# Kernel tuning notes

Measured on AMD Instinct MI355X. Metric: run time of the kernel, lower is better.

The kernel has to match this reference:

```python
import jax, jax.numpy as jnp
import numpy as np

NUM_USERS = 100000
USER_EMB_DIM = 64
PROC_DIM = 128          # Dense(128) embedding_processor
NUM_SHARDS = 16
MEM_SIZE = 512          # memory slots per shard
WORD_SIZE = 64
NUM_READS = 4
INPUT_SIZE = 256
B, S = 256, 128
IN_DIM = INPUT_SIZE + PROC_DIM  # combined controller input width


def setup_inputs() -> dict:
    key = jax.random.key(0)
    k = jax.random.split(key, 7)
    x = jax.random.normal(k[0], (B, S, INPUT_SIZE), dtype=jnp.float32)
    user_id = jax.random.randint(k[1], (B,), 0, NUM_USERS, dtype=jnp.int64)
    user_emb_table = jax.random.normal(k[2], (NUM_USERS, USER_EMB_DIM), dtype=jnp.float32) * 0.02
    W_proc = jax.random.normal(k[3], (USER_EMB_DIM, PROC_DIM), dtype=jnp.float32) * (1.0 / np.sqrt(USER_EMB_DIM))
    b_proc = jnp.zeros((PROC_DIM,), dtype=jnp.float32)
    # per-shard parameters: query projection + memory matrix (the shard's state)
    Wq = jax.random.normal(k[4], (NUM_SHARDS, IN_DIM, NUM_READS * WORD_SIZE), dtype=jnp.float32) * (1.0 / np.sqrt(IN_DIM))
    memory = jax.random.normal(k[5], (NUM_SHARDS, MEM_SIZE, WORD_SIZE), dtype=jnp.float32)
    return {"x": x, "user_id": user_id, "user_emb_table": user_emb_table,
            "W_proc": W_proc, "b_proc": b_proc, "Wq": Wq, "memory": memory}


def reference(x, user_id, user_emb_table, W_proc, b_proc, Wq, memory):
    # user embedding lookup + Dense processor
    ue = user_emb_table[user_id]                       # [B, E]
    pe = ue @ W_proc + b_proc                          # [B, PROC_DIM]
    # broadcast the processed embedding across the sequence and concat on features
    pe_seq = jnp.broadcast_to(pe[:, None, :], (x.shape[0], x.shape[1], pe.shape[-1]))
    combined = jnp.concatenate([x, pe_seq], axis=-1)   # [B, S, IN_DIM]
    # shard routing (irregular gather of per-shard params)
    sid = user_id % NUM_SHARDS                         # [B]
    Wq_g = Wq[sid]                                     # [B, IN_DIM, R*W]
    mem_g = memory[sid]                                # [B, M, W]
    # per-sample shard forward: content-based read
    q = jnp.einsum('bsi,bio->bso', combined, Wq_g)     # [B, S, R*W]
    q = q.reshape(q.shape[0], q.shape[1], NUM_READS, WORD_SIZE)
    scores = jnp.einsum('bsrw,bmw->bsrm', q, mem_g)    # [B, S, R, M]
    wts = jax.nn.softmax(scores, axis=-1)
    read_words = jnp.einsum('bsrm,bmw->bsrw', wts, mem_g)  # [B, S, R, W]
    # original code keeps final_states[-1] (last sample's state)
    final_state = wts[-1]                              # [S, R, M]
    return read_words, final_state
```

## Files before the change

### kernel.cpp

```cpp
#include <hip/hip_runtime.h>
#include <math.h>

#define BB 256
#define SSEQ 128
#define INPUT 256
#define PD 128
#define EE 64
#define RW 256
#define MM 512
#define WW 64
#define KD 384

typedef _Float16 half8 __attribute__((ext_vector_type(8)));
typedef __fp16 fp16x2 __attribute__((ext_vector_type(2)));
typedef float float4v __attribute__((ext_vector_type(4)));
typedef float f32x16 __attribute__((ext_vector_type(16)));
typedef unsigned int uint2v __attribute__((ext_vector_type(2)));

#define LOG2E 1.44269504088896f
#define OUT1 8388608u

#define MEMT16   4096
#define F32_OFF  131072
#define LDS_BYTES (131072 + 6144)
#define UE_O 0
#define PE_O 64
#define QPE_O 192
#define QP_O 448

union H8 { half8 h8; unsigned int u[4]; uint4 u4; };

__device__ __forceinline__ unsigned int pk2(float a, float b) {
    union { fp16x2 h; unsigned int u; } p;
    p.h = __builtin_amdgcn_cvt_pkrtz(a, b);
    return p.u;
}

__device__ __forceinline__ float xhalf_max(float v) {
    uint2v r = __builtin_amdgcn_permlane32_swap(__float_as_uint(v), __float_as_uint(v), false, false);
    return fmaxf(__uint_as_float(r[0]), __uint_as_float(r[1]));
}
__device__ __forceinline__ float xhalf_sum(float v) {
    uint2v r = __builtin_amdgcn_permlane32_swap(__float_as_uint(v), __float_as_uint(v), false, false);
    return __uint_as_float(r[0]) + __uint_as_float(r[1]);
}

__global__ void __launch_bounds__(1024, 4)
attn_kernel(const float* __restrict__ x, const int* __restrict__ user_id,
            const float* __restrict__ uet, const float* __restrict__ W_proc,
            const float* __restrict__ b_proc, const float* __restrict__ Wq,
            const float* __restrict__ memG, float* __restrict__ out)
{
    extern __shared__ char smraw[];
    unsigned short* smemu = (unsigned short*)smraw;
    unsigned int*   smw   = (unsigned int*)smraw;
    uint4*          sm128 = (uint4*)smraw;
    float*          smf   = (float*)(smraw + F32_OFF);

    const int t = threadIdx.x;
    const int b = blockIdx.x;
    const int lane = t & 63, wv = t >> 6;
    const int n16 = lane & 15, quad = lane >> 4;
    const int l31 = lane & 31, hh = lane >> 5;
    const int r = wv & 3, sq = wv >> 2;
    const int s0 = sq * 32;
    const int mswz = l31 & 7;

    const int uid = user_id[b];
    const int sid = uid & 15;
    const float* memB = memG + (size_t)sid * (MM*WW);
    const float* wqX  = Wq + (size_t)sid * KD * RW;

    if (t < EE) smf[UE_O + t] = uet[(size_t)uid*EE + t];

    {
        const int n = t & 255, h = t >> 8;
        for (int i = 0; i < 32; i += 4) {
            float w[8];
            #pragma unroll
            for (int j = 0; j < 4; ++j) {
                int kp = (i + j)*4 + h;
                w[2*j]   = wqX[(size_t)(2*kp)    *RW + n];
                w[2*j+1] = wqX[(size_t)(2*kp + 1)*RW + n];
            }
            #pragma unroll
            for (int j = 0; j < 4; ++j) {
                int kp = (i + j)*4 + h;
                smw[((((kp>>2)*256 + n) << 2) | (kp & 3))] = pk2(w[2*j], w[2*j+1]);
            }
        }
    }
    __syncthreads();

    if (t < PD) {
        float a = b_proc[t];
        #pragma unroll
        for (int e = 0; e < EE; ++e) a = fmaf(smf[UE_O + e], W_proc[e*PD + t], a);
        smf[PE_O + t] = a;
    }
    __syncthreads();
    {
        int n = t & 255, h = t >> 8;
        const float* wr = wqX + (size_t)(256 + h*32)*RW + n;
        float sa = 0.f, sb = 0.f, sc = 0.f, sd = 0.f;
        #pragma unroll
        for (int k = 0; k < 32; k += 4) {
            sa = fmaf(smf[PE_O + h*32 + k],     wr[(size_t)(k)*RW],     sa);
            sb = fmaf(smf[PE_O + h*32 + k + 1], wr[(size_t)(k + 1)*RW], sb);
            sc = fmaf(smf[PE_O + h*32 + k + 2], wr[(size_t)(k + 2)*RW], sc);
            sd = fmaf(smf[PE_O + h*32 + k + 3], wr[(size_t)(k + 3)*RW], sd);
        }
        smf[QP_O + h*256 + n] = (sa + sb) + (sc + sd);
    }
    __syncthreads();
    if (t < 256) smf[QPE_O + t] = LOG2E * (smf[QP_O + t] + smf[QP_O + 256 + t]
                                         + smf[QP_O + 512 + t] + smf[QP_O + 768 + t]);
    __syncthreads();

    float4v qacc[4][2];
    #pragma unroll
    for (int mt = 0; mt < 4; ++mt)
        #pragma unroll
        for (int nt = 0; nt < 2; ++nt) qacc[mt][nt] = (float4v)0.f;

    const float* xB = x + (size_t)(b*SSEQ + s0) * INPUT;
    for (int kc = 0; kc < 8; ++kc) {
        H8 afr[4];
        #pragma unroll
        for (int mt = 0; mt < 4; ++mt)
            afr[mt].u4 = sm128[(kc*4 + quad)*256 + r*64 + mt*16 + n16];
        H8 bfr[2];
        #pragma unroll
        for (int nt = 0; nt < 2; ++nt) {
            const float* xg = xB + (size_t)(nt*16 + n16)*INPUT + kc*32 + quad*8;
            float4 a0 = *(const float4*)xg;
            float4 a1 = *(const float4*)(xg + 4);
            bfr[nt].u[0] = pk2(a0.x*LOG2E, a0.y*LOG2E);
            bfr[nt].u[1] = pk2(a0.z*LOG2E, a0.w*LOG2E);
            bfr[nt].u[2] = pk2(a1.x*LOG2E, a1.y*LOG2E);
            bfr[nt].u[3] = pk2(a1.z*LOG2E, a1.w*LOG2E);
        }
        __builtin_amdgcn_s_setprio(1);
        #pragma unroll
        for (int mt = 0; mt < 4; ++mt)
            #pragma unroll
            for (int nt = 0; nt < 2; ++nt)
                qacc[mt][nt] = __builtin_amdgcn_mfma_f32_16x16x32_f16(afr[mt].h8, bfr[nt].h8, qacc[mt][nt], 0, 0, 0);
        __builtin_amdgcn_s_setprio(0);
    }
    #pragma unroll
    for (int mt = 0; mt < 4; ++mt)
        #pragma unroll
        for (int reg = 0; reg < 4; ++reg) {
            float qv = smf[QPE_O + r*64 + mt*16 + quad*4 + reg];
            #pragma unroll
            for (int nt = 0; nt < 2; ++nt) qacc[mt][nt][reg] += qv;
        }
    unsigned int pkq[4][2][2];
    #pragma unroll
    for (int mt = 0; mt < 4; ++mt)
        #pragma unroll
        for (int nt = 0; nt < 2; ++nt) {
            pkq[mt][nt][0] = pk2(qacc[mt][nt][0], qacc[mt][nt][1]);
            pkq[mt][nt][1] = pk2(qacc[mt][nt][2], qacc[mt][nt][3]);
        }
    H8 bqf[4];
    {
        const int ntSel = (lane >> 4) & 1;
        const int srcBase = (lane & 15) + (lane & 32);
        #pragma unroll
        for (int kc = 0; kc < 4; ++kc)
            #pragma unroll
            for (int jp = 0; jp < 4; ++jp) {
                const int src = srcBase + ((jp >> 1) << 4);
                int v0 = __shfl((int)pkq[kc][0][jp & 1], src, 64);
                int v1 = __shfl((int)pkq[kc][1][jp & 1], src, 64);
                bqf[kc].u[jp] = (unsigned int)(ntSel ? v1 : v0);
            }
    }
    __syncthreads();

    for (int i = 0; i < 4; ++i) {
        int id = t + i*1024;
        int m = id >> 3, cw = id & 7;
        const float* g = memB + m*64 + cw*8;
        float4 a0 = *(const float4*)g;
        float4 a1 = *(const float4*)(g + 4);
        sm128[m*8 + (cw ^ (m & 7))] =
            make_uint4(pk2(a0.x,a0.y), pk2(a0.z,a0.w), pk2(a1.x,a1.y), pk2(a1.z,a1.w));
    }
    __syncthreads();
    for (int i = 0; i < 4; ++i) {
        int id = t + i*1024;
        int w = id & 63, cm = id >> 6;
        unsigned int uu[4];
        #pragma unroll
        for (int p = 0; p < 4; ++p) {
            int m0 = cm*8 + 2*p, m1 = m0 + 1;
            unsigned short lo = smemu[m0*64 + (((w>>3) ^ (m0&7))<<3) + (w&7)];
            unsigned short hi = smemu[m1*64 + (((w>>3) ^ (m1&7))<<3) + (w&7)];
            uu[p] = (unsigned int)lo | ((unsigned int)hi << 16);
        }
        sm128[MEMT16 + w*64 + (cm ^ (w & 7))] = make_uint4(uu[0],uu[1],uu[2],uu[3]);
    }
    __syncthreads();

    if (sq == 1) __builtin_amdgcn_s_sleep(2);
    else if (sq == 2) __builtin_amdgcn_s_sleep(4);
    else if (sq == 3) __builtin_amdgcn_s_sleep(6);

    f32x16 Oa0 = (f32x16)0.f, Oa1 = (f32x16)0.f;
    float Ml = -1e30f, llp = 0.f;
    const int mt0 = sq * 4;

    H8 afc[4];
    #pragma unroll
    for (int kc = 0; kc < 4; ++kc)
        afc[kc].u4 = sm128[(mt0*32 + l31)*8 + (((kc<<1) + hh) ^ mswz)];

    for (int i = 0; i < 16; ++i) {
        const int mtile = (i + mt0) & 15;
        f32x16 Sa = (f32x16)0.f;
        __builtin_amdgcn_s_setprio(1);
        #pragma unroll
        for (int kc = 0; kc < 4; ++kc)
            Sa = __builtin_amdgcn_mfma_f32_32x32x16_f16(afc[kc].h8, bqf[kc].h8, Sa, 0, 0, 0);
        __builtin_amdgcn_s_setprio(0);
        if (i < 15) {
            const int mrow = ((i + 1 + mt0) & 15)*32 + l31;
            #pragma unroll
            for (int kc = 0; kc < 4; ++kc)
                afc[kc].u4 = sm128[mrow*8 + (((kc<<1) + hh) ^ mswz)];
        }
        const int c0 = mtile*4 + hh;
        H8 afP0, afP1, afP2, afP3;
        afP0.u4 = sm128[MEMT16 + l31*64        + ( c0      ^ mswz)];
        afP1.u4 = sm128[MEMT16 + l31*64        + ((c0 + 2) ^ mswz)];
        afP2.u4 = sm128[MEMT16 + (32 + l31)*64 + ( c0      ^ mswz)];
        afP3.u4 = sm128[MEMT16 + (32 + l31)*64 + ((c0 + 2) ^ mswz)];
        float m0 = fmaxf(fmaxf(Sa[0], Sa[1]), Sa[2]);
        float m1 = fmaxf(fmaxf(Sa[3], Sa[4]), Sa[5]);
        float m2 = fmaxf(fmaxf(Sa[6], Sa[7]), Sa[8]);
        float m3 = fmaxf(fmaxf(Sa[9], Sa[10]), Sa[11]);
        float m4 = fmaxf(fmaxf(Sa[12], Sa[13]), Sa[14]);
        float m5 = fmaxf(fmaxf(m0, m1), Sa[15]);
        float m6 = fmaxf(fmaxf(m2, m3), m4);
        float tmx = xhalf_max(fmaxf(m5, m6));
        if (__any(tmx > Ml + 8.0f)) {
            float Mn = fmaxf(Ml, tmx);
            float al = __builtin_amdgcn_exp2f(Ml - Mn);
            Ml = Mn;
            llp *= al;
            #pragma unroll
            for (int g = 0; g < 16; ++g) { Oa0[g] *= al; Oa1[g] *= al; }
        }
        float pv[16];
        #pragma unroll
        for (int g = 0; g < 16; ++g) pv[g] = __builtin_amdgcn_exp2f(Sa[g] - Ml);
        float ts = (((pv[0]+pv[1])+(pv[2]+pv[3])) + ((pv[4]+pv[5])+(pv[6]+pv[7])))
                 + (((pv[8]+pv[9])+(pv[10]+pv[11])) + ((pv[12]+pv[13])+(pv[14]+pv[15])));
        llp += ts;
        uint2v rA0 = __builtin_amdgcn_permlane32_swap(pk2(pv[0],pv[1]),   pk2(pv[4],pv[5]),   false, false);
        uint2v rB0 = __builtin_amdgcn_permlane32_swap(pk2(pv[2],pv[3]),   pk2(pv[6],pv[7]),   false, false);
        uint2v rA1 = __builtin_amdgcn_permlane32_swap(pk2(pv[8],pv[9]),   pk2(pv[12],pv[13]), false, false);
        uint2v rB1 = __builtin_amdgcn_permlane32_swap(pk2(pv[10],pv[11]), pk2(pv[14],pv[15]), false, false);
        H8 bp0; bp0.u[0]=rA0[0]; bp0.u[1]=rB0[0]; bp0.u[2]=rA0[1]; bp0.u[3]=rB0[1];
        H8 bp1; bp1.u[0]=rA1[0]; bp1.u[1]=rB1[0]; bp1.u[2]=rA1[1]; bp1.u[3]=rB1[1];
        __builtin_amdgcn_s_setprio(1);
        Oa0 = __builtin_amdgcn_mfma_f32_32x32x16_f16(afP0.h8, bp0.h8, Oa0, 0, 0, 0);
        Oa0 = __builtin_amdgcn_mfma_f32_32x32x16_f16(afP1.h8, bp1.h8, Oa0, 0, 0, 0);
        Oa1 = __builtin_amdgcn_mfma_f32_32x32x16_f16(afP2.h8, bp0.h8, Oa1, 0, 0, 0);
        Oa1 = __builtin_amdgcn_mfma_f32_32x32x16_f16(afP3.h8, bp1.h8, Oa1, 0, 0, 0);
        __builtin_amdgcn_s_setprio(0);
    }

    float inv = 1.0f / xhalf_sum(llp);

    {
        const int s = s0 + l31;
        float* op = out + ((size_t)(b*SSEQ + s)*4 + r)*WW;
        #pragma unroll
        for (int rq = 0; rq < 4; ++rq) {
            float4 o0 = make_float4(Oa0[rq*4+0]*inv, Oa0[rq*4+1]*inv,
                                    Oa0[rq*4+2]*inv, Oa0[rq*4+3]*inv);
            *(float4*)&op[rq*8 + hh*4] = o0;
            float4 o1 = make_float4(Oa1[rq*4+0]*inv, Oa1[rq*4+1]*inv,
                                    Oa1[rq*4+2]*inv, Oa1[rq*4+3]*inv);
            *(float4*)&op[32 + rq*8 + hh*4] = o1;
        }
    }

    if (b == BB - 1) {
        const int s = s0 + l31;
        size_t base = (size_t)OUT1 + ((size_t)(s*4 + r) << 9);
        for (int mtile = 0; mtile < 16; ++mtile) {
            f32x16 Sa = (f32x16)0.f;
            const int mrow = mtile*32 + l31;
            #pragma unroll
            for (int kc = 0; kc < 4; ++kc) {
                H8 af; af.u4 = sm128[mrow*8 + (((kc<<1) + hh) ^ mswz)];
                Sa = __builtin_amdgcn_mfma_f32_32x32x16_f16(af.h8, bqf[kc].h8, Sa, 0, 0, 0);
            }
            #pragma unroll
            for (int rq = 0; rq < 4; ++rq) {
                float4 w4 = make_float4(
                    __builtin_amdgcn_exp2f(Sa[rq*4+0] - Ml) * inv,
                    __builtin_amdgcn_exp2f(Sa[rq*4+1] - Ml) * inv,
                    __builtin_amdgcn_exp2f(Sa[rq*4+2] - Ml) * inv,
                    __builtin_amdgcn_exp2f(Sa[rq*4+3] - Ml) * inv);
                *(float4*)&out[base + mtile*32 + rq*8 + hh*4] = w4;
            }
        }
    }
}

extern "C" void kernel_launch(void* const* d_in, const int* in_sizes, int n_in,
                              void* d_out, int out_size, void* d_ws, size_t ws_size,
                              hipStream_t stream) {
    const float* x    = (const float*)d_in[0];
    const int*   uid  = (const int*)  d_in[1];
    const float* uet  = (const float*)d_in[2];
    const float* Wp   = (const float*)d_in[3];
    const float* bp   = (const float*)d_in[4];
    const float* Wq   = (const float*)d_in[5];
    const float* mem  = (const float*)d_in[6];
    float* out = (float*)d_out;

    (void)hipFuncSetAttribute((const void*)attn_kernel,
                              hipFuncAttributeMaxDynamicSharedMemorySize, LDS_BYTES);
    attn_kernel<<<BB, 1024, LDS_BYTES, stream>>>(x, uid, uet, Wp, bp, Wq, mem, out);
}
```

Before: 162.7 us.

## Store last block's softmax weights during main loop and rescale instead of recomputing

The last block now writes its unnormalized softmax probabilities and per-tile running max to the output and workspace during the main loop. Afterwards it rescales them in place using the final max and sum, which removes the second pass of score MFMAs and exp2 work that only block 255 did. The Wq staging loop is also rewritten to load eight consecutive rows per thread and store them as one 128-bit LDS write instead of four 32-bit scatter stores. The rescale path adds global read-modify-write traffic and falls back to the old recompute path when no workspace is provided.

```diff
diff --git a/kernel.cpp b/kernel.cpp
--- a/kernel.cpp
+++ b/kernel.cpp
@@ -49,11 +49,11 @@
 attn_kernel(const float* __restrict__ x, const int* __restrict__ user_id,
             const float* __restrict__ uet, const float* __restrict__ W_proc,
             const float* __restrict__ b_proc, const float* __restrict__ Wq,
-            const float* __restrict__ memG, float* __restrict__ out)
+            const float* __restrict__ memG, float* __restrict__ out,
+            float* __restrict__ wsf)
 {
     extern __shared__ char smraw[];
     unsigned short* smemu = (unsigned short*)smraw;
-    unsigned int*   smw   = (unsigned int*)smraw;
     uint4*          sm128 = (uint4*)smraw;
     float*          smf   = (float*)(smraw + F32_OFF);
 
@@ -75,19 +75,14 @@
 
     {
         const int n = t & 255, h = t >> 8;
-        for (int i = 0; i < 32; i += 4) {
+        for (int i = 0; i < 8; ++i) {
+            const int kb = i*4 + h;
+            const float* wr = wqX + (size_t)(8*kb)*RW + n;
             float w[8];
             #pragma unroll
-            for (int j = 0; j < 4; ++j) {
-                int kp = (i + j)*4 + h;
-                w[2*j]   = wqX[(size_t)(2*kp)    *RW + n];
-                w[2*j+1] = wqX[(size_t)(2*kp + 1)*RW + n];
-            }
-            #pragma unroll
-            for (int j = 0; j < 4; ++j) {
-                int kp = (i + j)*4 + h;
-                smw[((((kp>>2)*256 + n) << 2) | (kp & 3))] = pk2(w[2*j], w[2*j+1]);
-            }
+            for (int j = 0; j < 8; ++j) w[j] = wr[(size_t)j*RW];
+            sm128[kb*256 + n] =
+                make_uint4(pk2(w[0],w[1]), pk2(w[2],w[3]), pk2(w[4],w[5]), pk2(w[6],w[7]));
         }
     }
     __syncthreads();
@@ -212,6 +207,10 @@
     f32x16 Oa0 = (f32x16)0.f, Oa1 = (f32x16)0.f;
     float Ml = -1e30f, llp = 0.f;
     const int mt0 = sq * 4;
+    const bool dofix = (b == BB - 1) && (wsf != nullptr);
+    const int s = s0 + l31;
+    float* fsBase = out + (size_t)OUT1 + ((size_t)(s*4 + r) << 9);
+    float* mlBase = wsf ? (wsf + (size_t)wv*16*64 + lane) : nullptr;
 
     H8 afc[4];
     #pragma unroll
@@ -260,6 +259,14 @@
         float ts = (((pv[0]+pv[1])+(pv[2]+pv[3])) + ((pv[4]+pv[5])+(pv[6]+pv[7])))
                  + (((pv[8]+pv[9])+(pv[10]+pv[11])) + ((pv[12]+pv[13])+(pv[14]+pv[15])));
         llp += ts;
+        if (dofix) {
+            float* fp = fsBase + mtile*32 + hh*4;
+            *(float4*)(fp +  0) = make_float4(pv[0],  pv[1],  pv[2],  pv[3]);
+            *(float4*)(fp +  8) = make_float4(pv[4],  pv[5],  pv[6],  pv[7]);
+            *(float4*)(fp + 16) = make_float4(pv[8],  pv[9],  pv[10], pv[11]);
+            *(float4*)(fp + 24) = make_float4(pv[12], pv[13], pv[14], pv[15]);
+            mlBase[mtile*64] = Ml;
+        }
         uint2v rA0 = __builtin_amdgcn_permlane32_swap(pk2(pv[0],pv[1]),   pk2(pv[4],pv[5]),   false, false);
         uint2v rB0 = __builtin_amdgcn_permlane32_swap(pk2(pv[2],pv[3]),   pk2(pv[6],pv[7]),   false, false);
         uint2v rA1 = __builtin_amdgcn_permlane32_swap(pk2(pv[8],pv[9]),   pk2(pv[12],pv[13]), false, false);
@@ -277,7 +284,6 @@
     float inv = 1.0f / xhalf_sum(llp);
 
     {
-        const int s = s0 + l31;
         float* op = out + ((size_t)(b*SSEQ + s)*4 + r)*WW;
         #pragma unroll
         for (int rq = 0; rq < 4; ++rq) {
@@ -290,8 +296,20 @@
         }
     }
 
-    if (b == BB - 1) {
-        const int s = s0 + l31;
+    if (dofix) {
+        asm volatile("s_waitcnt vmcnt(0) lgkmcnt(0)" ::: "memory");
+        for (int mtile = 0; mtile < 16; ++mtile) {
+            float mlog = mlBase[mtile*64];
+            float scale = __builtin_amdgcn_exp2f(mlog - Ml) * inv;
+            float* fp = fsBase + mtile*32 + hh*4;
+            #pragma unroll
+            for (int rq = 0; rq < 4; ++rq) {
+                float4 v = *(float4*)(fp + rq*8);
+                v.x *= scale; v.y *= scale; v.z *= scale; v.w *= scale;
+                *(float4*)(fp + rq*8) = v;
+            }
+        }
+    } else if (b == BB - 1) {
         size_t base = (size_t)OUT1 + ((size_t)(s*4 + r) << 9);
         for (int mtile = 0; mtile < 16; ++mtile) {
             f32x16 Sa = (f32x16)0.f;
@@ -325,8 +343,9 @@
     const float* Wq   = (const float*)d_in[5];
     const float* mem  = (const float*)d_in[6];
     float* out = (float*)d_out;
+    float* wsf = (d_ws != nullptr && ws_size >= 65536) ? (float*)d_ws : nullptr;
 
     (void)hipFuncSetAttribute((const void*)attn_kernel,
                               hipFuncAttributeMaxDynamicSharedMemorySize, LDS_BYTES);
-    attn_kernel<<<BB, 1024, LDS_BYTES, stream>>>(x, uid, uet, Wp, bp, Wq, mem, out);
-}
+    attn_kernel<<<BB, 1024, LDS_BYTES, stream>>>(x, uid, uet, Wp, bp, Wq, mem, out, wsf);
+}
```

Measured after the change: 219.3 us. 34.8% more time.
